# Kernel optimization log

Hardware: AMD Instinct MI355X
Metric: run time of the kernel (lower is better)

Reference implementation:

```python
import jax, jax.numpy as jnp
import numpy as np

EMBED_DIM = 1024
NUM_HEADS = 16
HEAD_DIM = EMBED_DIM // NUM_HEADS


def setup_inputs() -> dict:
    key = jax.random.key(0)
    ks = jax.random.split(key, 6)
    B, S, D = 4, 2048, EMBED_DIM
    std = 1.0 / np.sqrt(D)
    x = jax.random.normal(ks[0], (B, S, D), dtype=jnp.float32)
    wq = jax.random.normal(ks[1], (D, D), dtype=jnp.float32) * std
    wk = jax.random.normal(ks[2], (D, D), dtype=jnp.float32) * std
    wv = jax.random.normal(ks[3], (D, D), dtype=jnp.float32) * std
    wo = jax.random.normal(ks[4], (D, D), dtype=jnp.float32) * std
    bo = jax.random.normal(ks[5], (D,), dtype=jnp.float32) * 0.01
    return {"x": x, "wq": wq, "wk": wk, "wv": wv, "wo": wo, "bo": bo}


def reference(x, wq, wk, wv, wo, bo):
    B, S, D = x.shape
    H, Hd = NUM_HEADS, HEAD_DIM
    scale = 1.0 / jnp.sqrt(jnp.asarray(Hd, x.dtype))
    # nn.Linear computes x @ W.T; split into heads -> [B, H, S, Hd]
    q = (x @ wq.T).reshape(B, S, H, Hd).transpose(0, 2, 1, 3)
    k = (x @ wk.T).reshape(B, S, H, Hd).transpose(0, 2, 1, 3)
    v = (x @ wv.T).reshape(B, S, H, Hd).transpose(0, 2, 1, 3)
    scores = jnp.einsum("bhqd,bhkd->bhqk", q, k) * scale  # [B,H,S,S]
    attn = jax.nn.softmax(scores, axis=-1)
    ctx = jnp.einsum("bhqk,bhkd->bhqd", attn, v)
    ctx = ctx.transpose(0, 2, 1, 3).reshape(B, S, D)
    return ctx @ wo.T + bo
```

## Files before the change

### kernel.cpp

```cpp
#include <hip/hip_runtime.h>

typedef __bf16 bf16x8 __attribute__((ext_vector_type(8)));
typedef float f32x4 __attribute__((ext_vector_type(4)));
typedef unsigned u32x4 __attribute__((ext_vector_type(4)));
typedef unsigned short u16;

#define GAS __attribute__((address_space(1)))
#define LAS __attribute__((address_space(3)))

static __device__ __forceinline__ void gload16(const void* g, void* l) {
  __builtin_amdgcn_global_load_lds((const GAS unsigned int*)g, (LAS unsigned int*)l, 16, 0, 0);
}

static __device__ __forceinline__ u16 f2bf(float f) {
  unsigned u = __builtin_bit_cast(unsigned, f);
  u += 0x7fffu + ((u >> 16) & 1u);
  return (u16)(u >> 16);
}

static __device__ __forceinline__ unsigned pk2(float lo, float hi) {
  ushort2 u;
  u.x = __builtin_bit_cast(u16, (__bf16)lo);
  u.y = __builtin_bit_cast(u16, (__bf16)hi);
  return __builtin_bit_cast(unsigned, u);
}

__global__ void cvt_all(const float* __restrict__ x, const float* __restrict__ wq,
                        const float* __restrict__ wk, const float* __restrict__ wv,
                        const float* __restrict__ wo, u16* __restrict__ xb,
                        u16* __restrict__ wqkvb, u16* __restrict__ wob) {
  int i = blockIdx.x * 256 + threadIdx.x;
  float4 v;
  ushort4* dst;
  if (i < 2097152) {
    v = reinterpret_cast<const float4*>(x)[i];
    dst = reinterpret_cast<ushort4*>(xb) + i;
  } else if (i < 2883584) {
    int j = i - 2097152;
    const float* s = j < 262144 ? wq : (j < 524288 ? wk : wv);
    int jj = j < 262144 ? j : (j < 524288 ? j - 262144 : j - 524288);
    v = reinterpret_cast<const float4*>(s)[jj];
    dst = reinterpret_cast<ushort4*>(wqkvb) + j;
  } else {
    int j = i - 2883584;
    v = reinterpret_cast<const float4*>(wo)[j];
    dst = reinterpret_cast<ushort4*>(wob) + j;
  }
  ushort4 o;
  o.x = f2bf(v.x); o.y = f2bf(v.y); o.z = f2bf(v.z); o.w = f2bf(v.w);
  *dst = o;
}

__global__ void gemm_qkv(const u16* __restrict__ A, const u16* __restrict__ W,
                         u16* __restrict__ Qo, u16* __restrict__ Ko, u16* __restrict__ Vo) {
  __shared__ u16 As[2 * 128 * 32];
  __shared__ u16 Bs[2 * 128 * 32];
  const int t = threadIdx.x;
  const int lane = t & 63;
  const int w = t >> 6;
  const int wr = w >> 1, wc = w & 1;
  const int l15 = lane & 15, lhi = lane >> 4;
  const int swz = (blockIdx.x & 7) * 192 + (blockIdx.x >> 3);
  const int bm = swz / 24, bn = swz % 24;

  f32x4 acc[4][4];
#pragma unroll
  for (int a = 0; a < 4; ++a)
#pragma unroll
    for (int b = 0; b < 4; ++b) acc[a][b] = (f32x4){0.f, 0.f, 0.f, 0.f};

  const u16* ag = A + (size_t)(bm * 128 + (t >> 2)) * 1024 + (t & 3) * 8;
  const u16* bg = W + (size_t)(bn * 128 + (t >> 2)) * 1024 + (t & 3) * 8;

  auto stage = [&](int cb, int kt) {
    gload16(ag + kt * 32, &As[cb + t * 8]);
    gload16(ag + kt * 32 + 64 * 1024, &As[cb + t * 8 + 2048]);
    gload16(bg + kt * 32, &Bs[cb + t * 8]);
    gload16(bg + kt * 32 + 64 * 1024, &Bs[cb + t * 8 + 2048]);
  };

  stage(0, 0);
  asm volatile("s_waitcnt vmcnt(0)" ::: "memory");
  __builtin_amdgcn_s_barrier();

  for (int kt = 0; kt < 32; ++kt) {
    const int cb = (kt & 1) * 4096;
    if (kt < 31) stage(cb ^ 4096, kt + 1);
    bf16x8 af[4], bfr[4];
#pragma unroll
    for (int mt = 0; mt < 4; ++mt)
      af[mt] = *(const bf16x8*)&As[cb + (wr * 64 + mt * 16 + l15) * 32 + lhi * 8];
#pragma unroll
    for (int nt = 0; nt < 4; ++nt)
      bfr[nt] = *(const bf16x8*)&Bs[cb + (wc * 64 + nt * 16 + l15) * 32 + lhi * 8];
#pragma unroll
    for (int mt = 0; mt < 4; ++mt)
#pragma unroll
      for (int nt = 0; nt < 4; ++nt)
        acc[mt][nt] = __builtin_amdgcn_mfma_f32_16x16x32_bf16(af[mt], bfr[nt], acc[mt][nt], 0, 0, 0);
    asm volatile("s_waitcnt vmcnt(0)" ::: "memory");
    __builtin_amdgcn_s_barrier();
  }

  const int tsel = bn >> 3;
  const int m0 = bm * 128 + wr * 64;
  const int n0 = bn * 128 + wc * 64;
  const int bb = bm >> 4;
  if (tsel == 0) {
    const float qs = 0.125f * 1.4426950408889634f;
#pragma unroll
    for (int nt = 0; nt < 4; ++nt) {
      int n = n0 + nt * 16 + l15;
      int c = n & 1023, h = c >> 6, hd = c & 63;
      size_t base = (size_t)(bb * 16 + h) * 2048 * 64 + hd;
#pragma unroll
      for (int mt = 0; mt < 4; ++mt)
#pragma unroll
        for (int i = 0; i < 4; ++i) {
          int s = (m0 + mt * 16 + lhi * 4 + i) & 2047;
          Qo[base + (size_t)s * 64] = f2bf(acc[mt][nt][i] * qs);
        }
    }
  } else if (tsel == 1) {
#pragma unroll
    for (int nt = 0; nt < 4; ++nt) {
      int n = n0 + nt * 16 + l15;
      int c = n & 1023, h = c >> 6, hd = c & 63;
      size_t base = (size_t)(bb * 16 + h) * 2048 * 64 + hd;
#pragma unroll
      for (int mt = 0; mt < 4; ++mt)
#pragma unroll
        for (int i = 0; i < 4; ++i) {
          int s = (m0 + mt * 16 + lhi * 4 + i) & 2047;
          Ko[base + (size_t)s * 64] = f2bf(acc[mt][nt][i]);
        }
    }
  } else {
#pragma unroll
    for (int nt = 0; nt < 4; ++nt) {
      int n = n0 + nt * 16 + l15;
      int c = n & 1023, h = c >> 6, hd = c & 63;
#pragma unroll
      for (int mt = 0; mt < 4; ++mt) {
        int s0 = (m0 + mt * 16 + lhi * 4) & 2047;
        int sp0 = ((s0 >> 4) & 1) * 4 + ((s0 >> 2) & 3) * 8 + (s0 >> 5) * 32;
        ushort4 pk;
        pk.x = f2bf(acc[mt][nt][0]);
        pk.y = f2bf(acc[mt][nt][1]);
        pk.z = f2bf(acc[mt][nt][2]);
        pk.w = f2bf(acc[mt][nt][3]);
        *(ushort4*)&Vo[((size_t)(bb * 16 + h) * 64 + hd) * 2048 + sp0] = pk;
      }
    }
  }
}

__global__ __launch_bounds__(256, 4) void attn_kernel(const u16* __restrict__ Q,
                                                      const u16* __restrict__ K,
                                                      const u16* __restrict__ Vp,
                                                      u16* __restrict__ Ctx) {
  __shared__ u16 Ks[2 * 64 * 64];
  __shared__ u16 Vs[2 * 64 * 64];
  const int t = threadIdx.x;
  const int lane = t & 63;
  const int w = t >> 6;
  const int l15 = lane & 15, lhi = lane >> 4;
  const int swz = (blockIdx.x & 7) * 256 + (blockIdx.x >> 3);
  const int qt = swz & 31, pair = swz >> 5;
  const u16* qp = Q + (size_t)pair * 2048 * 64;
  const u16* kp = K + (size_t)pair * 2048 * 64;
  const u16* vp = Vp + (size_t)pair * 64 * 2048;

  const int qrow = qt * 64 + w * 16 + l15;
  bf16x8 qf0 = *(const bf16x8*)&qp[(size_t)qrow * 64 + lhi * 8];
  bf16x8 qf1 = *(const bf16x8*)&qp[(size_t)qrow * 64 + 32 + lhi * 8];

  const u32x4 ow = {0x3F803F80u, 0x3F803F80u, 0x3F803F80u, 0x3F803F80u};
  const bf16x8 onesf = __builtin_bit_cast(bf16x8, ow);

  const int swzq = (l15 & 7) << 3;
  const int kofs0 = l15 * 64 + ((lhi * 8) ^ swzq);
  const int kofs1 = l15 * 64 + ((32 + lhi * 8) ^ swzq);
  const int vofs0 = l15 * 64 + ((lhi * 8) ^ swzq);
  const int vofs1 = l15 * 64 + ((32 + lhi * 8) ^ swzq);

  f32x4 co[4], la;
  la = (f32x4){0.f, 0.f, 0.f, 0.f};
#pragma unroll
  for (int n = 0; n < 4; ++n) co[n] = la;

  auto stage = [&](int cb, int tt) {
#pragma unroll
    for (int j = 0; j < 2; ++j) {
      int c = j * 256 + t;
      int r = c >> 3, c8 = (c & 7) * 8;
      gload16(kp + (size_t)(tt * 64 + r) * 64 + (c8 ^ ((r & 7) << 3)), &Ks[cb + c * 8]);
    }
#pragma unroll
    for (int j = 0; j < 2; ++j) {
      int c = j * 256 + t;
      int r = c >> 3, c8 = (c & 7) * 8;
      gload16(vp + (size_t)r * 2048 + tt * 64 + (c8 ^ ((r & 7) << 3)), &Vs[cb + c * 8]);
    }
  };

  stage(0, 0);
  asm volatile("s_waitcnt vmcnt(0)" ::: "memory");
  __builtin_amdgcn_s_barrier();

  for (int kt = 0; kt < 32; ++kt) {
    const int cb = (kt & 1) * 4096;
    if (kt < 31) stage(cb ^ 4096, kt + 1);

    f32x4 sa[4];
    __builtin_amdgcn_s_setprio(1);
#pragma unroll
    for (int nt = 0; nt < 4; ++nt) {
      bf16x8 kf0 = *(const bf16x8*)&Ks[cb + kofs0 + nt * 1024];
      bf16x8 kf1 = *(const bf16x8*)&Ks[cb + kofs1 + nt * 1024];
      f32x4 z = (f32x4){0.f, 0.f, 0.f, 0.f};
      z = __builtin_amdgcn_mfma_f32_16x16x32_bf16(kf0, qf0, z, 0, 0, 0);
      sa[nt] = __builtin_amdgcn_mfma_f32_16x16x32_bf16(kf1, qf1, z, 0, 0, 0);
    }
    __builtin_amdgcn_s_setprio(0);

#pragma unroll
    for (int nt = 0; nt < 4; ++nt)
#pragma unroll
      for (int e = 0; e < 4; ++e) sa[nt][e] = __builtin_exp2f(sa[nt][e]);
    unsigned pw[4][2];
#pragma unroll
    for (int nt = 0; nt < 4; ++nt) {
      pw[nt][0] = pk2(sa[nt][0], sa[nt][1]);
      pw[nt][1] = pk2(sa[nt][2], sa[nt][3]);
    }

    __builtin_amdgcn_s_setprio(1);
#pragma unroll
    for (int ks = 0; ks < 2; ++ks) {
      u32x4 aw = {pw[2 * ks][0], pw[2 * ks][1], pw[2 * ks + 1][0], pw[2 * ks + 1][1]};
      bf16x8 af = __builtin_bit_cast(bf16x8, aw);
      la = __builtin_amdgcn_mfma_f32_16x16x32_bf16(af, onesf, la, 0, 0, 0);
      const int vo = ks ? vofs1 : vofs0;
#pragma unroll
      for (int nthd = 0; nthd < 4; ++nthd) {
        bf16x8 vf = *(const bf16x8*)&Vs[cb + vo + nthd * 1024];
        co[nthd] = __builtin_amdgcn_mfma_f32_16x16x32_bf16(af, vf, co[nthd], 0, 0, 0);
      }
    }
    __builtin_amdgcn_s_setprio(0);

    asm volatile("s_waitcnt vmcnt(0)" ::: "memory");
    __builtin_amdgcn_s_barrier();
  }

  float li[4];
#pragma unroll
  for (int i = 0; i < 4; ++i) li[i] = 1.0f / la[i];
  const int bb = pair >> 4, hh = pair & 15;
  const int sbase = qt * 64 + w * 16 + lhi * 4;
#pragma unroll
  for (int nthd = 0; nthd < 4; ++nthd) {
    int hd = nthd * 16 + l15;
#pragma unroll
    for (int i = 0; i < 4; ++i)
      Ctx[(size_t)(bb * 2048 + sbase + i) * 1024 + hh * 64 + hd] = f2bf(co[nthd][i] * li[i]);
  }
}

__global__ void gemm_out(const u16* __restrict__ A, const u16* __restrict__ W,
                         const float* __restrict__ Bo, float* __restrict__ Out) {
  __shared__ u16 As[2 * 128 * 32];
  __shared__ u16 Bs[2 * 128 * 32];
  const int t = threadIdx.x;
  const int lane = t & 63;
  const int w = t >> 6;
  const int wr = w >> 1, wc = w & 1;
  const int l15 = lane & 15, lhi = lane >> 4;
  const int swz = (blockIdx.x & 7) * 64 + (blockIdx.x >> 3);
  const int bm = swz >> 3, bn = swz & 7;

  f32x4 acc[4][4];
#pragma unroll
  for (int a = 0; a < 4; ++a)
#pragma unroll
    for (int b = 0; b < 4; ++b) acc[a][b] = (f32x4){0.f, 0.f, 0.f, 0.f};

  const u16* ag = A + (size_t)(bm * 128 + (t >> 2)) * 1024 + (t & 3) * 8;
  const u16* bg = W + (size_t)(bn * 128 + (t >> 2)) * 1024 + (t & 3) * 8;

  auto stage = [&](int cb, int kt) {
    gload16(ag + kt * 32, &As[cb + t * 8]);
    gload16(ag + kt * 32 + 64 * 1024, &As[cb + t * 8 + 2048]);
    gload16(bg + kt * 32, &Bs[cb + t * 8]);
    gload16(bg + kt * 32 + 64 * 1024, &Bs[cb + t * 8 + 2048]);
  };

  stage(0, 0);
  asm volatile("s_waitcnt vmcnt(0)" ::: "memory");
  __builtin_amdgcn_s_barrier();

  for (int kt = 0; kt < 32; ++kt) {
    const int cb = (kt & 1) * 4096;
    if (kt < 31) stage(cb ^ 4096, kt + 1);
    bf16x8 af[4], bfr[4];
#pragma unroll
    for (int mt = 0; mt < 4; ++mt)
      af[mt] = *(const bf16x8*)&As[cb + (wr * 64 + mt * 16 + l15) * 32 + lhi * 8];
#pragma unroll
    for (int nt = 0; nt < 4; ++nt)
      bfr[nt] = *(const bf16x8*)&Bs[cb + (wc * 64 + nt * 16 + l15) * 32 + lhi * 8];
#pragma unroll
    for (int mt = 0; mt < 4; ++mt)
#pragma unroll
      for (int nt = 0; nt < 4; ++nt)
        acc[mt][nt] = __builtin_amdgcn_mfma_f32_16x16x32_bf16(af[mt], bfr[nt], acc[mt][nt], 0, 0, 0);
    asm volatile("s_waitcnt vmcnt(0)" ::: "memory");
    __builtin_amdgcn_s_barrier();
  }

  const int m0 = bm * 128 + wr * 64;
  const int n0 = bn * 128 + wc * 64;
#pragma unroll
  for (int nt = 0; nt < 4; ++nt) {
    int n = n0 + nt * 16 + l15;
    float bias = Bo[n];
#pragma unroll
    for (int mt = 0; mt < 4; ++mt)
#pragma unroll
      for (int i = 0; i < 4; ++i) {
        int m = m0 + mt * 16 + lhi * 4 + i;
        Out[(size_t)m * 1024 + n] = acc[mt][nt][i] + bias;
      }
  }
}

extern "C" void kernel_launch(void* const* d_in, const int* in_sizes, int n_in,
                              void* d_out, int out_size, void* d_ws, size_t ws_size,
                              hipStream_t stream) {
  const float* x  = (const float*)d_in[0];
  const float* wq = (const float*)d_in[1];
  const float* wk = (const float*)d_in[2];
  const float* wv = (const float*)d_in[3];
  const float* wo = (const float*)d_in[4];
  const float* bo = (const float*)d_in[5];
  float* out = (float*)d_out;

  u16* xb    = (u16*)d_ws;
  u16* wqkvb = xb + (size_t)8 * 1024 * 1024;
  u16* wob   = wqkvb + (size_t)3 * 1024 * 1024;
  u16* qb    = wob + (size_t)1 * 1024 * 1024;
  u16* kb    = qb + (size_t)8 * 1024 * 1024;
  u16* vtb   = kb + (size_t)8 * 1024 * 1024;
  u16* ctxb  = xb;

  cvt_all<<<12288, 256, 0, stream>>>(x, wq, wk, wv, wo, xb, wqkvb, wob);
  gemm_qkv<<<64 * 24, 256, 0, stream>>>(xb, wqkvb, qb, kb, vtb);
  attn_kernel<<<2048, 256, 0, stream>>>(qb, kb, vtb, ctxb);
  gemm_out<<<64 * 8, 256, 0, stream>>>(ctxb, wob, bo, out);
}
```

Measured before the change: 224.1 us.

## Give each attention wave four query sub-tiles to reuse K/V fragments

```diff
diff --git a/kernel.cpp b/kernel.cpp
--- a/kernel.cpp
+++ b/kernel.cpp
@@ -155,7 +155,7 @@
   }
 }
 
-__global__ __launch_bounds__(256, 4) void attn_kernel(const u16* __restrict__ Q,
+__global__ __launch_bounds__(128, 2) void attn_kernel(const u16* __restrict__ Q,
                                                       const u16* __restrict__ K,
                                                       const u16* __restrict__ Vp,
                                                       u16* __restrict__ Ctx) {
@@ -165,15 +165,19 @@
   const int lane = t & 63;
   const int w = t >> 6;
   const int l15 = lane & 15, lhi = lane >> 4;
-  const int swz = (blockIdx.x & 7) * 256 + (blockIdx.x >> 3);
-  const int qt = swz & 31, pair = swz >> 5;
+  const int swz = (blockIdx.x & 7) * 128 + (blockIdx.x >> 3);
+  const int qt = swz & 15, pair = swz >> 4;
   const u16* qp = Q + (size_t)pair * 2048 * 64;
   const u16* kp = K + (size_t)pair * 2048 * 64;
   const u16* vp = Vp + (size_t)pair * 64 * 2048;
 
-  const int qrow = qt * 64 + w * 16 + l15;
-  bf16x8 qf0 = *(const bf16x8*)&qp[(size_t)qrow * 64 + lhi * 8];
-  bf16x8 qf1 = *(const bf16x8*)&qp[(size_t)qrow * 64 + 32 + lhi * 8];
+  const int qr0 = qt * 128 + w * 64 + l15;
+  bf16x8 qf[4][2];
+#pragma unroll
+  for (int s = 0; s < 4; ++s) {
+    qf[s][0] = *(const bf16x8*)&qp[(size_t)(qr0 + s * 16) * 64 + lhi * 8];
+    qf[s][1] = *(const bf16x8*)&qp[(size_t)(qr0 + s * 16) * 64 + 32 + lhi * 8];
+  }
 
   const u32x4 ow = {0x3F803F80u, 0x3F803F80u, 0x3F803F80u, 0x3F803F80u};
   const bf16x8 onesf = __builtin_bit_cast(bf16x8, ow);
@@ -181,24 +185,26 @@
   const int swzq = (l15 & 7) << 3;
   const int kofs0 = l15 * 64 + ((lhi * 8) ^ swzq);
   const int kofs1 = l15 * 64 + ((32 + lhi * 8) ^ swzq);
-  const int vofs0 = l15 * 64 + ((lhi * 8) ^ swzq);
-  const int vofs1 = l15 * 64 + ((32 + lhi * 8) ^ swzq);
-
-  f32x4 co[4], la;
-  la = (f32x4){0.f, 0.f, 0.f, 0.f};
-#pragma unroll
-  for (int n = 0; n < 4; ++n) co[n] = la;
+  const int vofs0 = kofs0, vofs1 = kofs1;
+
+  f32x4 co[4][4], la[4];
+#pragma unroll
+  for (int s = 0; s < 4; ++s) {
+    la[s] = (f32x4){0.f, 0.f, 0.f, 0.f};
+#pragma unroll
+    for (int n = 0; n < 4; ++n) co[s][n] = la[s];
+  }
 
   auto stage = [&](int cb, int tt) {
 #pragma unroll
-    for (int j = 0; j < 2; ++j) {
-      int c = j * 256 + t;
+    for (int j = 0; j < 4; ++j) {
+      int c = j * 128 + t;
       int r = c >> 3, c8 = (c & 7) * 8;
       gload16(kp + (size_t)(tt * 64 + r) * 64 + (c8 ^ ((r & 7) << 3)), &Ks[cb + c * 8]);
     }
 #pragma unroll
-    for (int j = 0; j < 2; ++j) {
-      int c = j * 256 + t;
+    for (int j = 0; j < 4; ++j) {
+      int c = j * 128 + t;
       int r = c >> 3, c8 = (c & 7) * 8;
       gload16(vp + (size_t)r * 2048 + tt * 64 + (c8 ^ ((r & 7) << 3)), &Vs[cb + c * 8]);
     }
@@ -212,40 +218,52 @@
     const int cb = (kt & 1) * 4096;
     if (kt < 31) stage(cb ^ 4096, kt + 1);
 
-    f32x4 sa[4];
+    f32x4 sa[4][4];
     __builtin_amdgcn_s_setprio(1);
 #pragma unroll
     for (int nt = 0; nt < 4; ++nt) {
       bf16x8 kf0 = *(const bf16x8*)&Ks[cb + kofs0 + nt * 1024];
       bf16x8 kf1 = *(const bf16x8*)&Ks[cb + kofs1 + nt * 1024];
-      f32x4 z = (f32x4){0.f, 0.f, 0.f, 0.f};
-      z = __builtin_amdgcn_mfma_f32_16x16x32_bf16(kf0, qf0, z, 0, 0, 0);
-      sa[nt] = __builtin_amdgcn_mfma_f32_16x16x32_bf16(kf1, qf1, z, 0, 0, 0);
+#pragma unroll
+      for (int s = 0; s < 4; ++s) {
+        f32x4 z = (f32x4){0.f, 0.f, 0.f, 0.f};
+        z = __builtin_amdgcn_mfma_f32_16x16x32_bf16(kf0, qf[s][0], z, 0, 0, 0);
+        sa[s][nt] = __builtin_amdgcn_mfma_f32_16x16x32_bf16(kf1, qf[s][1], z, 0, 0, 0);
+      }
     }
     __builtin_amdgcn_s_setprio(0);
 
-#pragma unroll
-    for (int nt = 0; nt < 4; ++nt)
-#pragma unroll
-      for (int e = 0; e < 4; ++e) sa[nt][e] = __builtin_exp2f(sa[nt][e]);
-    unsigned pw[4][2];
-#pragma unroll
-    for (int nt = 0; nt < 4; ++nt) {
-      pw[nt][0] = pk2(sa[nt][0], sa[nt][1]);
-      pw[nt][1] = pk2(sa[nt][2], sa[nt][3]);
+    unsigned pw[4][4][2];
+#pragma unroll
+    for (int s = 0; s < 4; ++s) {
+#pragma unroll
+      for (int nt = 0; nt < 4; ++nt)
+#pragma unroll
+        for (int e = 0; e < 4; ++e) sa[s][nt][e] = __builtin_exp2f(sa[s][nt][e]);
+#pragma unroll
+      for (int nt = 0; nt < 4; ++nt) {
+        pw[s][nt][0] = pk2(sa[s][nt][0], sa[s][nt][1]);
+        pw[s][nt][1] = pk2(sa[s][nt][2], sa[s][nt][3]);
+      }
     }
 
     __builtin_amdgcn_s_setprio(1);
 #pragma unroll
     for (int ks = 0; ks < 2; ++ks) {
-      u32x4 aw = {pw[2 * ks][0], pw[2 * ks][1], pw[2 * ks + 1][0], pw[2 * ks + 1][1]};
-      bf16x8 af = __builtin_bit_cast(bf16x8, aw);
-      la = __builtin_amdgcn_mfma_f32_16x16x32_bf16(af, onesf, la, 0, 0, 0);
       const int vo = ks ? vofs1 : vofs0;
-#pragma unroll
-      for (int nthd = 0; nthd < 4; ++nthd) {
-        bf16x8 vf = *(const bf16x8*)&Vs[cb + vo + nthd * 1024];
-        co[nthd] = __builtin_amdgcn_mfma_f32_16x16x32_bf16(af, vf, co[nthd], 0, 0, 0);
+      bf16x8 vf[4];
+#pragma unroll
+      for (int nthd = 0; nthd < 4; ++nthd)
+        vf[nthd] = *(const bf16x8*)&Vs[cb + vo + nthd * 1024];
+#pragma unroll
+      for (int s = 0; s < 4; ++s) {
+        u32x4 aw = {pw[s][2 * ks][0], pw[s][2 * ks][1],
+                    pw[s][2 * ks + 1][0], pw[s][2 * ks + 1][1]};
+        bf16x8 af = __builtin_bit_cast(bf16x8, aw);
+        la[s] = __builtin_amdgcn_mfma_f32_16x16x32_bf16(af, onesf, la[s], 0, 0, 0);
+#pragma unroll
+        for (int nthd = 0; nthd < 4; ++nthd)
+          co[s][nthd] = __builtin_amdgcn_mfma_f32_16x16x32_bf16(af, vf[nthd], co[s][nthd], 0, 0, 0);
       }
     }
     __builtin_amdgcn_s_setprio(0);
@@ -254,17 +272,21 @@
     __builtin_amdgcn_s_barrier();
   }
 
-  float li[4];
-#pragma unroll
-  for (int i = 0; i < 4; ++i) li[i] = 1.0f / la[i];
   const int bb = pair >> 4, hh = pair & 15;
-  const int sbase = qt * 64 + w * 16 + lhi * 4;
-#pragma unroll
-  for (int nthd = 0; nthd < 4; ++nthd) {
-    int hd = nthd * 16 + l15;
-#pragma unroll
-    for (int i = 0; i < 4; ++i)
-      Ctx[(size_t)(bb * 2048 + sbase + i) * 1024 + hh * 64 + hd] = f2bf(co[nthd][i] * li[i]);
+#pragma unroll
+  for (int s = 0; s < 4; ++s) {
+    float li[4];
+#pragma unroll
+    for (int i = 0; i < 4; ++i) li[i] = 1.0f / la[s][i];
+    const int sbase = qt * 128 + w * 64 + s * 16 + lhi * 4;
+#pragma unroll
+    for (int nthd = 0; nthd < 4; ++nthd) {
+      int hd = nthd * 16 + l15;
+#pragma unroll
+      for (int i = 0; i < 4; ++i)
+        Ctx[(size_t)(bb * 2048 + sbase + i) * 1024 + hh * 64 + hd] =
+            f2bf(co[s][nthd][i] * li[i]);
+    }
   }
 }
 
@@ -356,6 +378,6 @@
 
   cvt_all<<<12288, 256, 0, stream>>>(x, wq, wk, wv, wo, xb, wqkvb, wob);
   gemm_qkv<<<64 * 24, 256, 0, stream>>>(xb, wqkvb, qb, kb, vtb);
-  attn_kernel<<<2048, 256, 0, stream>>>(qb, kb, vtb, ctxb);
+  attn_kernel<<<1024, 128, 0, stream>>>(qb, kb, vtb, ctxb);
   gemm_out<<<64 * 8, 256, 0, stream>>>(ctxb, wob, bo, out);
 }
```

Measured after the change: 223.3 us. Within noise of the previous version (-0.4%).
